# Kernel tuning notes

Hardware: AMD Instinct MI355X
Metric: run time of the kernel (lower is better)

Reference implementation:

```python
import jax, jax.numpy as jnp
import numpy as np

B, D, C, E, K = 4096, 784, 10, 1024, 8   # batch, input_size, num_classes, num_classifiers, k_neighbors
TANH_FACTOR = 10.0
EPS = 1e-12


def setup_inputs() -> dict:
    key = jax.random.key(0)
    ks = jax.random.split(key, 8)
    x = jax.random.normal(ks[0], (B, D), dtype=jnp.float32)
    keys_raw = jax.random.normal(ks[1], (E, D), dtype=jnp.float32)
    keys = keys_raw / jnp.maximum(jnp.linalg.norm(keys_raw, axis=1, keepdims=True), EPS)
    # weak-learner weights (VarianceScaling fan_in ~ 1/sqrt(D)) and biases
    Wm = jax.random.normal(ks[2], (E, C, D), dtype=jnp.float32) / jnp.sqrt(D)
    bm = jnp.zeros((E, C), dtype=jnp.float32)
    # vanilla classifier (scale=0.1 -> std ~ sqrt(0.1/D))
    Wv = jax.random.normal(ks[3], (C, D), dtype=jnp.float32) * jnp.sqrt(0.1 / D)
    bv = jnp.zeros((C,), dtype=jnp.float32)
    # tanh classifier
    Wt = jax.random.normal(ks[4], (C, D), dtype=jnp.float32) * jnp.sqrt(0.1 / D)
    bt = jnp.zeros((C,), dtype=jnp.float32)
    return {"x": x, "keys": keys, "Wm": Wm, "bm": bm, "Wv": Wv, "bv": bv, "Wt": Wt, "bt": bt}


def reference(x, keys, Wm, bm, Wv, bv, Wt, bt):
    # --- lookup_memory: cosine-similarity routing (keys are pre-normalized) ---
    xn = x / jnp.maximum(jnp.linalg.norm(x, axis=1, keepdims=True), EPS)  # l2 normalize
    cos = xn @ keys.T                       # [B, E]
    sims, idx = jax.lax.top_k(cos, K)       # descending similarity, [B, K]
    # Faithful to torch: experts are gathered in ascending model-index order
    # (enumerate over ModuleList), while weights `sims` stay similarity-sorted.
    gidx = jnp.sort(idx, axis=1)            # [B, K]

    # --- ensemble_forward: gather expert weights, per-sample tiny GEMVs ---
    Wg = Wm[gidx]                           # [B, K, C, D] (irregular gather)
    bg = bm[gidx]                           # [B, K, C]
    expert_raw = jnp.einsum('bd,bkcd->bkc', x, Wg) + bg
    expert_out = jnp.tanh(expert_raw / TANH_FACTOR) * TANH_FACTOR
    w = sims[..., None]                     # [B, K, 1]
    ensemble = jnp.sum(expert_out * w, axis=1) / jnp.sum(w, axis=1)  # [B, C]

    # --- vanilla / tanh classifiers ---
    vanilla = jax.nn.log_softmax(x @ Wv.T + bv, axis=1)
    tanh_out = jnp.tanh((x @ Wt.T + bt) / TANH_FACTOR) * TANH_FACTOR
    return ensemble, tanh_out, vanilla
```

## Files before the change

### kernel.cpp

```cpp
#include <hip/hip_runtime.h>
#include <hip/hip_bf16.h>
#include <math.h>

#define B_ 4096
#define D_ 784
#define C_ 10
#define E_ 1024
#define K_ 8
#define KP 832
#define KH 416
#define CHR 104
#define NW 1088
#define LDR 72
#define CAP 48
#define ECAP 128
#define MARG 0.04f

typedef float f32x4 __attribute__((ext_vector_type(4)));
typedef short s16x8 __attribute__((ext_vector_type(8)));

__device__ __forceinline__ float wave_reduce_sum(float v) {
  #pragma unroll
  for (int off = 32; off > 0; off >>= 1) v += __shfl_xor(v, off, 64);
  return v;
}

__device__ __forceinline__ float bitonic64_f(float v, int lane) {
  #pragma unroll
  for (int k = 2; k <= 64; k <<= 1)
    #pragma unroll
    for (int j = k >> 1; j > 0; j >>= 1) {
      float o = __shfl_xor(v, j, 64);
      bool keepmin = ((lane & j) == 0) == ((lane & k) == 0);
      v = keepmin ? fminf(v, o) : fmaxf(v, o);
    }
  return v;
}

__device__ __forceinline__ unsigned long long bitonic64_u(unsigned long long v, int lane) {
  #pragma unroll
  for (int k = 2; k <= 64; k <<= 1)
    #pragma unroll
    for (int j = k >> 1; j > 0; j >>= 1) {
      unsigned long long o = __shfl_xor(v, j, 64);
      bool keepmin = ((lane & j) == 0) == ((lane & k) == 0);
      v = keepmin ? (v < o ? v : o) : (v < o ? o : v);
    }
  return v;
}

__device__ __forceinline__ unsigned long long packkey(float v, int idx) {
  unsigned ub = __float_as_uint(v);
  ub = (ub & 0x80000000u) ? ~ub : (ub | 0x80000000u);
  return ((unsigned long long)ub << 32) | (unsigned)(~idx);
}
__device__ __forceinline__ float unpackval(unsigned long long k) {
  unsigned ub = (unsigned)(k >> 32);
  unsigned fb = (ub & 0x80000000u) ? (ub ^ 0x80000000u) : ~ub;
  return __uint_as_float(fb);
}

__global__ __launch_bounds__(256) void prep_all(const float* __restrict__ x,
                                                const float* __restrict__ keys,
                                                const float* __restrict__ Wv,
                                                const float* __restrict__ Wt,
                                                unsigned short* __restrict__ xh,
                                                unsigned short* __restrict__ kh,
                                                float* __restrict__ out_ens,
                                                int* __restrict__ count) {
  int gt = blockIdx.x * 256 + threadIdx.x;
  if (gt < E_) count[gt] = 0;
  int t = gt;
  const float* src = nullptr;
  unsigned short* dst;
  if (t < B_ * CHR) {
    int row = t / CHR, ch = t % CHR;
    dst = xh + (size_t)row * KP + ch * 8;
    src = (ch < 98) ? x + (size_t)row * D_ + ch * 8 : nullptr;
  } else {
    t -= B_ * CHR;
    if (t < NW * CHR) {
      int row = t / CHR, ch = t % CHR;
      dst = kh + (size_t)row * KP + ch * 8;
      if (ch < 98) {
        if (row < E_) src = keys + (size_t)row * D_ + ch * 8;
        else if (row < E_ + 10) src = Wv + (size_t)(row - E_) * D_ + ch * 8;
        else if (row < E_ + 20) src = Wt + (size_t)(row - E_ - 10) * D_ + ch * 8;
      }
    } else {
      t -= NW * CHR;
      if (t < (B_ * C_) / 4) {
        float4 z = make_float4(0.f, 0.f, 0.f, 0.f);
        ((float4*)out_ens)[t] = z;
      }
      return;
    }
  }
  unsigned short u[8];
  if (src) {
    #pragma unroll
    for (int i = 0; i < 8; ++i) {
      __hip_bfloat16 h = __float2bfloat16(src[i]);
      u[i] = *(unsigned short*)&h;
    }
  } else {
    #pragma unroll
    for (int i = 0; i < 8; ++i) u[i] = 0;
  }
  *(uint4*)dst = *(uint4*)u;
}

__global__ __launch_bounds__(256) void gemm_bf16(const unsigned short* __restrict__ xh,
                                                 const unsigned short* __restrict__ kh,
                                                 float* __restrict__ cosb) {
  __shared__ unsigned short As[64 * LDR];
  __shared__ unsigned short Bs[64 * LDR];
  const int tid  = threadIdx.x;
  const int bid  = blockIdx.y * 17 + blockIdx.x;
  const int swz  = (bid & 7) * 136 + (bid >> 3);
  const int row0 = (swz / 17) * 64, col0 = (swz % 17) * 64;
  const int srow = tid >> 2, sq = tid & 3;
  const int lane = tid & 63, w = tid >> 6;
  const int wr = (w >> 1) * 32, wc = (w & 1) * 32;
  const int fr = lane & 15, fg = lane >> 4;

  const unsigned short* gx = xh + (size_t)(row0 + srow) * KP;
  const unsigned short* gk = kh + (size_t)(col0 + srow) * KP;
  unsigned short* sa = As + srow * LDR + sq * 8;
  unsigned short* sb = Bs + srow * LDR + sq * 8;
  const unsigned short* pa0 = As + (wr + fr) * LDR + fg * 8;
  const unsigned short* pb0 = Bs + (wc + fr) * LDR + fg * 8;

  uint4 va0 = *(const uint4*)(gx + sq * 8);
  uint4 va1 = *(const uint4*)(gx + 32 + sq * 8);
  uint4 vb0 = *(const uint4*)(gk + sq * 8);
  uint4 vb1 = *(const uint4*)(gk + 32 + sq * 8);

  f32x4 acc[2][2] = {};
  for (int t = 0; t < 13; ++t) {
    __syncthreads();
    *(uint4*)sa = va0; *(uint4*)(sa + 32) = va1;
    *(uint4*)sb = vb0; *(uint4*)(sb + 32) = vb1;
    __syncthreads();
    if (t < 12) {
      int k1 = (t + 1) * 64;
      va0 = *(const uint4*)(gx + k1 + sq * 8);
      va1 = *(const uint4*)(gx + k1 + 32 + sq * 8);
      vb0 = *(const uint4*)(gk + k1 + sq * 8);
      vb1 = *(const uint4*)(gk + k1 + 32 + sq * 8);
    }
    #pragma unroll
    for (int kk = 0; kk < 64; kk += 32) {
      s16x8 a0 = *(const s16x8*)(pa0 + kk);
      s16x8 a1 = *(const s16x8*)(pa0 + 16 * LDR + kk);
      s16x8 b0 = *(const s16x8*)(pb0 + kk);
      s16x8 b1 = *(const s16x8*)(pb0 + 16 * LDR + kk);
      acc[0][0] = __builtin_amdgcn_mfma_f32_16x16x32_bf16(a0, b0, acc[0][0], 0, 0, 0);
      acc[0][1] = __builtin_amdgcn_mfma_f32_16x16x32_bf16(a0, b1, acc[0][1], 0, 0, 0);
      acc[1][0] = __builtin_amdgcn_mfma_f32_16x16x32_bf16(a1, b0, acc[1][0], 0, 0, 0);
      acc[1][1] = __builtin_amdgcn_mfma_f32_16x16x32_bf16(a1, b1, acc[1][1], 0, 0, 0);
    }
  }
  #pragma unroll
  for (int m = 0; m < 2; ++m)
    #pragma unroll
    for (int n = 0; n < 2; ++n)
      #pragma unroll
      for (int j = 0; j < 4; ++j) {
        int r = row0 + wr + m * 16 + fg * 4 + j;
        int c = col0 + wc + n * 16 + fr;
        cosb[(size_t)r * NW + c] = acc[m][n][j];
      }
}

__global__ __launch_bounds__(256) void topk_select(const float* __restrict__ cosb,
                                                   const float* __restrict__ x,
                                                   const float* __restrict__ keys,
                                                   const float* __restrict__ bv,
                                                   const float* __restrict__ bt,
                                                   float* __restrict__ sims,
                                                   int* __restrict__ count,
                                                   int* __restrict__ list,
                                                   float* __restrict__ out_tanh,
                                                   float* __restrict__ out_van) {
  __shared__ unsigned long long sKey[4][CAP];
  const int tid = threadIdx.x, w = tid >> 6, lane = tid & 63;
  const int row = (blockIdx.x << 2) + w;
  const float* cr = cosb + (size_t)row * NW;

  {
    float hv = (lane < 20) ? cr[E_ + lane] : 0.f;
    float vv = 0.f, tv = 0.f;
    if (lane < 10) vv = hv + bv[lane];
    else if (lane < 20) tv = hv + bt[lane - 10];
    float mv = (lane < 10) ? vv : -__builtin_inff();
    #pragma unroll
    for (int off = 1; off < 16; off <<= 1) mv = fmaxf(mv, __shfl_xor(mv, off, 64));
    float ev = (lane < 10) ? expf(vv - mv) : 0.f;
    float se = ev;
    #pragma unroll
    for (int off = 1; off < 16; off <<= 1) se += __shfl_xor(se, off, 64);
    if (lane < 10) out_van[(size_t)row * C_ + lane] = vv - (mv + logf(se));
    else if (lane < 20) out_tanh[(size_t)row * C_ + (lane - 10)] = tanhf(tv * 0.1f) * 10.0f;
  }

  float vals[16];
  #pragma unroll
  for (int j = 0; j < 16; ++j) vals[j] = cr[j * 64 + lane];
  float lm = vals[0];
  #pragma unroll
  for (int j = 1; j < 16; ++j) lm = fmaxf(lm, vals[j]);

  float srt = bitonic64_f(lm, lane);
  const float thr = __shfl(srt, 56) - MARG;

  int cnt = 0;
  #pragma unroll
  for (int j = 0; j < 16; ++j) {
    bool p = vals[j] >= thr;
    unsigned long long mk = __ballot(p);
    if (p) {
      int pos = cnt + __popcll(mk & ((1ull << lane) - 1ull));
      if (pos < CAP) sKey[w][pos] = packkey(vals[j], j * 64 + lane);
    }
    cnt += __popcll(mk);
  }
  const int m = cnt < CAP ? cnt : CAP;

  unsigned long long key = (lane < m) ? sKey[w][lane] : 0ull;
  key = bitonic64_u(key, lane);

  const float a8 = unpackval(__shfl(key, 56));
  const float a9 = unpackval(__shfl(key, 55));

  if (a8 - a9 <= MARG) {
    const float4* xp4 = (const float4*)(x + (size_t)row * D_);
    float4 xr[4];
    #pragma unroll
    for (int i = 0; i < 3; ++i) xr[i] = xp4[i * 64 + lane];
    xr[3] = make_float4(0.f, 0.f, 0.f, 0.f);
    if (lane < 4) xr[3] = xp4[192 + lane];

    float myv = unpackval(key);
    unsigned long long rm = __ballot(key != 0ull && fabsf(myv - a8) <= MARG);
    while (rm) {
      int L = __builtin_ctzll(rm);
      rm &= rm - 1;
      unsigned long long kL = __shfl(key, L);
      int ei = (int)(~(unsigned)kL) & (E_ - 1);
      const float4* kp4 = (const float4*)(keys + (size_t)ei * D_);
      float s = 0.f;
      #pragma unroll
      for (int i = 0; i < 3; ++i) {
        float4 kv = kp4[i * 64 + lane];
        s += xr[i].x * kv.x + xr[i].y * kv.y + xr[i].z * kv.z + xr[i].w * kv.w;
      }
      if (lane < 4) {
        float4 kv = kp4[192 + lane];
        s += xr[3].x * kv.x + xr[3].y * kv.y + xr[3].z * kv.z + xr[3].w * kv.w;
      }
      s = wave_reduce_sum(s);
      if (lane == L) key = packkey(s, ei);
    }
    key = bitonic64_u(key, lane);
  }

  if (lane >= 56) {
    float simv = unpackval(key);
    int ei = (int)(~(unsigned)key) & (E_ - 1);
    float ssum = simv;
    ssum += __shfl_xor(ssum, 1, 64);
    ssum += __shfl_xor(ssum, 2, 64);
    ssum += __shfl_xor(ssum, 4, 64);
    sims[row * K_ + (63 - lane)] = simv / ssum;
    int si = ei;
    const int l3 = lane & 7;
    #pragma unroll
    for (int k = 2; k <= 8; k <<= 1) {
      #pragma unroll
      for (int j = k >> 1; j > 0; j >>= 1) {
        int o = __shfl_xor(si, j, 64);
        bool lower = (l3 & j) == 0;
        bool asc = (l3 & k) == 0;
        int mn = si < o ? si : o;
        int mx = si < o ? o : si;
        si = (lower == asc) ? mn : mx;
      }
    }
    int pos = atomicAdd(&count[si], 1);
    if (pos < ECAP) list[si * ECAP + pos] = row * K_ + (lane - 56);
  }
}

__global__ __launch_bounds__(256) void expert_mfma(const float* __restrict__ Wm,
                                                   const float* __restrict__ bm,
                                                   const unsigned short* __restrict__ xh,
                                                   const int* __restrict__ list,
                                                   const int* __restrict__ count,
                                                   const float* __restrict__ sims,
                                                   float* __restrict__ out_ens) {
  __shared__ float cmb[2][16][17];
  const int e   = blockIdx.x;
  const int tid = threadIdx.x;
  int n = count[e];
  n = n < ECAP ? n : ECAP;
  if (n == 0) return;
  const int base = e * ECAP;

  const int lane = tid & 63, w = tid >> 6;
  const int g   = w >> 1;
  const int kh2 = w & 1;
  const int fr = lane & 15, fg = lane >> 4;
  const float bias = (fr < C_) ? bm[e * C_ + fr] : 0.f;

  s16x8 bfrag[13];
  #pragma unroll
  for (int c = 0; c < 13; ++c) {
    int kb = kh2 * KH + c * 32 + fg * 8;
    s16x8 bb = {0, 0, 0, 0, 0, 0, 0, 0};
    if (fr < C_ && kb < 784) {
      const float4* s4 = (const float4*)(Wm + (size_t)e * (C_ * D_) + fr * D_ + kb);
      float4 f0 = s4[0], f1 = s4[1];
      __hip_bfloat16 h;
      h = __float2bfloat16(f0.x); bb[0] = *(short*)&h;
      h = __float2bfloat16(f0.y); bb[1] = *(short*)&h;
      h = __float2bfloat16(f0.z); bb[2] = *(short*)&h;
      h = __float2bfloat16(f0.w); bb[3] = *(short*)&h;
      h = __float2bfloat16(f1.x); bb[4] = *(short*)&h;
      h = __float2bfloat16(f1.y); bb[5] = *(short*)&h;
      h = __float2bfloat16(f1.z); bb[6] = *(short*)&h;
      h = __float2bfloat16(f1.w); bb[7] = *(short*)&h;
    }
    bfrag[c] = bb;
  }

  for (int c0b = 0; c0b < n; c0b += 32) {
    const int c0 = c0b + g * 16;
    int sidx = c0 + fr;
    int item = (sidx < n) ? list[base + sidx] : list[base];
    const unsigned short* xrow = xh + (size_t)(item >> 3) * KP + kh2 * KH + fg * 8;
    f32x4 acc = {};
    #pragma unroll
    for (int c = 0; c < 13; ++c) {
      s16x8 a = *(const s16x8*)(xrow + c * 32);
      acc = __builtin_amdgcn_mfma_f32_16x16x32_bf16(a, bfrag[c], acc, 0, 0, 0);
    }
    if (kh2 == 1) {
      #pragma unroll
      for (int j = 0; j < 4; ++j) cmb[g][fg * 4 + j][fr] = acc[j];
    }
    __syncthreads();
    if (kh2 == 0 && fr < C_) {
      #pragma unroll
      for (int j = 0; j < 4; ++j) {
        int s2 = c0 + fg * 4 + j;
        if (s2 < n) {
          int it2 = list[base + s2];
          float sum = acc[j] + cmb[g][fg * 4 + j][fr];
          float val = tanhf((sum + bias) * 0.1f) * 10.0f;
          atomicAdd(&out_ens[(size_t)(it2 >> 3) * C_ + fr], val * sims[it2]);
        }
      }
    }
    __syncthreads();
  }
}

extern "C" void kernel_launch(void* const* d_in, const int* in_sizes, int n_in,
                              void* d_out, int out_size, void* d_ws, size_t ws_size,
                              hipStream_t stream) {
  const float* x    = (const float*)d_in[0];
  const float* keys = (const float*)d_in[1];
  const float* Wm   = (const float*)d_in[2];
  const float* bm   = (const float*)d_in[3];
  const float* Wv   = (const float*)d_in[4];
  const float* bv   = (const float*)d_in[5];
  const float* Wt   = (const float*)d_in[6];
  const float* bt   = (const float*)d_in[7];
  float* out = (float*)d_out;
  float* out_ens  = out;
  float* out_tanh = out + (size_t)B_ * C_;
  float* out_van  = out + 2 * (size_t)B_ * C_;

  char* p = (char*)d_ws;
  auto carve = [&](size_t bytes) { char* q = p; p += (bytes + 255) & ~(size_t)255; return q; };
  float* cosb  = (float*)carve((size_t)B_ * NW * 4);
  float* sims  = (float*)carve(B_ * K_ * 4);
  unsigned short* xh = (unsigned short*)carve((size_t)B_ * KP * 2);
  unsigned short* kh = (unsigned short*)carve((size_t)NW * KP * 2);
  int*   count  = (int*)carve(E_ * 4);
  int*   list   = (int*)carve((size_t)E_ * ECAP * 4);

  int prep_threads = B_ * CHR + NW * CHR + (B_ * C_) / 4;
  prep_all<<<(prep_threads + 255) / 256, 256, 0, stream>>>(x, keys, Wv, Wt, xh, kh,
                                                           out_ens, count);
  dim3 g(NW / 64, B_ / 64);
  gemm_bf16<<<g, 256, 0, stream>>>(xh, kh, cosb);
  topk_select<<<B_ / 4, 256, 0, stream>>>(cosb, x, keys, bv, bt, sims, count, list,
                                          out_tanh, out_van);
  expert_mfma<<<E_, 256, 0, stream>>>(Wm, bm, xh, list, count, sims, out_ens);
}
```

Measured before the change: 73.95 us.

## Replace threshold-filter top-k with per-lane sort and butterfly merge network

Top-k selection used to take each lane's max, bitonic-sort those maxima across the wave to get a threshold, compact the candidates into shared memory and then run a 64-wide bitonic sort on 64-bit keys. Now each lane sorts its 16 candidates in registers, and six xor-shuffle merge rounds keep the top 16 across the wave, so every lane ends up holding the global sorted top-16. This drops the shared-memory compaction, the CAP overflow limit and two full wave-wide bitonic sorts. In exchange it costs many more register compare-swaps and 16 64-bit shuffles per round, which raises register pressure. The refinement loop is also now uniform across the wave and runs over the register array.

After: 97.91 us. 32.4% more time.

```diff
diff --git a/kernel.cpp b/kernel.cpp
--- a/kernel.cpp
+++ b/kernel.cpp
@@ -12,7 +12,6 @@
 #define CHR 104
 #define NW 1088
 #define LDR 72
-#define CAP 48
 #define ECAP 128
 #define MARG 0.04f
 
@@ -22,30 +21,6 @@
 __device__ __forceinline__ float wave_reduce_sum(float v) {
   #pragma unroll
   for (int off = 32; off > 0; off >>= 1) v += __shfl_xor(v, off, 64);
-  return v;
-}
-
-__device__ __forceinline__ float bitonic64_f(float v, int lane) {
-  #pragma unroll
-  for (int k = 2; k <= 64; k <<= 1)
-    #pragma unroll
-    for (int j = k >> 1; j > 0; j >>= 1) {
-      float o = __shfl_xor(v, j, 64);
-      bool keepmin = ((lane & j) == 0) == ((lane & k) == 0);
-      v = keepmin ? fminf(v, o) : fmaxf(v, o);
-    }
-  return v;
-}
-
-__device__ __forceinline__ unsigned long long bitonic64_u(unsigned long long v, int lane) {
-  #pragma unroll
-  for (int k = 2; k <= 64; k <<= 1)
-    #pragma unroll
-    for (int j = k >> 1; j > 0; j >>= 1) {
-      unsigned long long o = __shfl_xor(v, j, 64);
-      bool keepmin = ((lane & j) == 0) == ((lane & k) == 0);
-      v = keepmin ? (v < o ? v : o) : (v < o ? o : v);
-    }
   return v;
 }
 
@@ -58,6 +33,23 @@
   unsigned ub = (unsigned)(k >> 32);
   unsigned fb = (ub & 0x80000000u) ? (ub ^ 0x80000000u) : ~ub;
   return __uint_as_float(fb);
+}
+
+__device__ __forceinline__ void sort16_desc(unsigned long long (&a)[16]) {
+  #pragma unroll
+  for (int k = 2; k <= 16; k <<= 1)
+    #pragma unroll
+    for (int j = k >> 1; j > 0; j >>= 1)
+      #pragma unroll
+      for (int i = 0; i < 16; ++i) {
+        int l = i ^ j;
+        if (l > i) {
+          bool desc = ((i & k) == 0);
+          unsigned long long x = a[i], y = a[l];
+          bool sw = desc ? (x < y) : (x > y);
+          if (sw) { a[i] = y; a[l] = x; }
+        }
+      }
 }
 
 __global__ __launch_bounds__(256) void prep_all(const float* __restrict__ x,
@@ -183,7 +175,6 @@
                                                    int* __restrict__ list,
                                                    float* __restrict__ out_tanh,
                                                    float* __restrict__ out_van) {
-  __shared__ unsigned long long sKey[4][CAP];
   const int tid = threadIdx.x, w = tid >> 6, lane = tid & 63;
   const int row = (blockIdx.x << 2) + w;
   const float* cr = cosb + (size_t)row * NW;
@@ -204,34 +195,36 @@
     else if (lane < 20) out_tanh[(size_t)row * C_ + (lane - 10)] = tanhf(tv * 0.1f) * 10.0f;
   }
 
-  float vals[16];
-  #pragma unroll
-  for (int j = 0; j < 16; ++j) vals[j] = cr[j * 64 + lane];
-  float lm = vals[0];
-  #pragma unroll
-  for (int j = 1; j < 16; ++j) lm = fmaxf(lm, vals[j]);
-
-  float srt = bitonic64_f(lm, lane);
-  const float thr = __shfl(srt, 56) - MARG;
-
-  int cnt = 0;
-  #pragma unroll
-  for (int j = 0; j < 16; ++j) {
-    bool p = vals[j] >= thr;
-    unsigned long long mk = __ballot(p);
-    if (p) {
-      int pos = cnt + __popcll(mk & ((1ull << lane) - 1ull));
-      if (pos < CAP) sKey[w][pos] = packkey(vals[j], j * 64 + lane);
-    }
-    cnt += __popcll(mk);
-  }
-  const int m = cnt < CAP ? cnt : CAP;
-
-  unsigned long long key = (lane < m) ? sKey[w][lane] : 0ull;
-  key = bitonic64_u(key, lane);
-
-  const float a8 = unpackval(__shfl(key, 56));
-  const float a9 = unpackval(__shfl(key, 55));
+  unsigned long long key[16];
+  #pragma unroll
+  for (int j = 0; j < 16; ++j) key[j] = packkey(cr[j * 64 + lane], j * 64 + lane);
+  sort16_desc(key);
+
+  #pragma unroll
+  for (int r = 0; r < 6; ++r) {
+    const int off = 1 << r;
+    unsigned long long c[16];
+    #pragma unroll
+    for (int i = 0; i < 16; ++i) {
+      unsigned long long o = __shfl_xor(key[15 - i], off, 64);
+      c[i] = key[i] > o ? key[i] : o;
+    }
+    #pragma unroll
+    for (int j = 8; j > 0; j >>= 1)
+      #pragma unroll
+      for (int i = 0; i < 16; ++i)
+        if ((i & j) == 0) {
+          int l = i | j;
+          unsigned long long xk = c[i], yk = c[l];
+          c[i] = xk > yk ? xk : yk;
+          c[l] = xk > yk ? yk : xk;
+        }
+    #pragma unroll
+    for (int i = 0; i < 16; ++i) key[i] = c[i];
+  }
+
+  const float a8 = unpackval(key[7]);
+  const float a9 = unpackval(key[8]);
 
   if (a8 - a9 <= MARG) {
     const float4* xp4 = (const float4*)(x + (size_t)row * D_);
@@ -241,54 +234,55 @@
     xr[3] = make_float4(0.f, 0.f, 0.f, 0.f);
     if (lane < 4) xr[3] = xp4[192 + lane];
 
-    float myv = unpackval(key);
-    unsigned long long rm = __ballot(key != 0ull && fabsf(myv - a8) <= MARG);
-    while (rm) {
-      int L = __builtin_ctzll(rm);
-      rm &= rm - 1;
-      unsigned long long kL = __shfl(key, L);
-      int ei = (int)(~(unsigned)kL) & (E_ - 1);
-      const float4* kp4 = (const float4*)(keys + (size_t)ei * D_);
-      float s = 0.f;
-      #pragma unroll
-      for (int i = 0; i < 3; ++i) {
-        float4 kv = kp4[i * 64 + lane];
-        s += xr[i].x * kv.x + xr[i].y * kv.y + xr[i].z * kv.z + xr[i].w * kv.w;
-      }
-      if (lane < 4) {
-        float4 kv = kp4[192 + lane];
-        s += xr[3].x * kv.x + xr[3].y * kv.y + xr[3].z * kv.z + xr[3].w * kv.w;
-      }
-      s = wave_reduce_sum(s);
-      if (lane == L) key = packkey(s, ei);
-    }
-    key = bitonic64_u(key, lane);
-  }
-
-  if (lane >= 56) {
-    float simv = unpackval(key);
-    int ei = (int)(~(unsigned)key) & (E_ - 1);
-    float ssum = simv;
-    ssum += __shfl_xor(ssum, 1, 64);
-    ssum += __shfl_xor(ssum, 2, 64);
-    ssum += __shfl_xor(ssum, 4, 64);
-    sims[row * K_ + (63 - lane)] = simv / ssum;
-    int si = ei;
-    const int l3 = lane & 7;
-    #pragma unroll
-    for (int k = 2; k <= 8; k <<= 1) {
-      #pragma unroll
-      for (int j = k >> 1; j > 0; j >>= 1) {
-        int o = __shfl_xor(si, j, 64);
-        bool lower = (l3 & j) == 0;
-        bool asc = (l3 & k) == 0;
-        int mn = si < o ? si : o;
-        int mx = si < o ? o : si;
-        si = (lower == asc) ? mn : mx;
-      }
-    }
-    int pos = atomicAdd(&count[si], 1);
-    if (pos < ECAP) list[si * ECAP + pos] = row * K_ + (lane - 56);
+    #pragma unroll
+    for (int j = 0; j < 16; ++j) {
+      float vj = unpackval(key[j]);
+      if (fabsf(vj - a8) <= MARG) {
+        int ei = (int)(~(unsigned)key[j]) & (E_ - 1);
+        const float4* kp4 = (const float4*)(keys + (size_t)ei * D_);
+        float s = 0.f;
+        #pragma unroll
+        for (int i = 0; i < 3; ++i) {
+          float4 kv = kp4[i * 64 + lane];
+          s += xr[i].x * kv.x + xr[i].y * kv.y + xr[i].z * kv.z + xr[i].w * kv.w;
+        }
+        if (lane < 4) {
+          float4 kv = kp4[192 + lane];
+          s += xr[3].x * kv.x + xr[3].y * kv.y + xr[3].z * kv.z + xr[3].w * kv.w;
+        }
+        s = wave_reduce_sum(s);
+        key[j] = packkey(s, ei);
+      }
+    }
+    sort16_desc(key);
+  }
+
+  float ssum = 0.f;
+  #pragma unroll
+  for (int j = 0; j < K_; ++j) ssum += unpackval(key[j]);
+
+  int id8[K_];
+  #pragma unroll
+  for (int j = 0; j < K_; ++j) id8[j] = (int)(~(unsigned)key[j]) & (E_ - 1);
+  #define CSWAP(a, b) { int lo = id8[a] < id8[b] ? id8[a] : id8[b]; \
+                        int hi = id8[a] < id8[b] ? id8[b] : id8[a]; \
+                        id8[a] = lo; id8[b] = hi; }
+  CSWAP(0,1) CSWAP(2,3) CSWAP(4,5) CSWAP(6,7)
+  CSWAP(0,2) CSWAP(1,3) CSWAP(4,6) CSWAP(5,7)
+  CSWAP(1,2) CSWAP(5,6)
+  CSWAP(0,4) CSWAP(1,5) CSWAP(2,6) CSWAP(3,7)
+  CSWAP(2,4) CSWAP(3,5)
+  CSWAP(1,2) CSWAP(3,4) CSWAP(5,6)
+  #undef CSWAP
+
+  if (lane < K_) {
+    float myv = 0.f; int myid = 0;
+    #pragma unroll
+    for (int j = 0; j < K_; ++j)
+      if (lane == j) { myv = unpackval(key[j]); myid = id8[j]; }
+    sims[row * K_ + lane] = myv / ssum;
+    int pos = atomicAdd(&count[myid], 1);
+    if (pos < ECAP) list[myid * ECAP + pos] = row * K_ + lane;
   }
 }
 
```
